# Optimization experiments

Hardware: AMD Instinct MI355X
Metric: run time of the kernel (lower is better)

Reference implementation:

```python
import jax, jax.numpy as jnp
import numpy as np

N = 100_000   # nodes
E = 1_600_000 # edges
IN, HID, OUT = 128, 64, 32


def _glorot(key, fan_in, fan_out):
    s = jnp.sqrt(6.0 / (fan_in + fan_out)).astype(jnp.float32)
    return jax.random.uniform(key, (fan_in, fan_out), jnp.float32, -s, s)


def setup_inputs() -> dict:
    key = jax.random.key(0)
    ks = jax.random.split(key, 8)
    x = jax.random.normal(ks[0], (N, IN), jnp.float32)
    edge_index = jax.random.randint(ks[1], (2, E), 0, N, jnp.int64)
    return {
        "x": x,
        "edge_index": edge_index,
        "W1": _glorot(ks[2], IN, HID),
        "b1": jnp.zeros((HID,), jnp.float32),
        "W_mu": _glorot(ks[3], HID, OUT),
        "b_mu": jnp.zeros((OUT,), jnp.float32),
        "W_ls": _glorot(ks[4], HID, OUT),
        "b_ls": jnp.zeros((OUT,), jnp.float32),
    }


def _gcn_conv(x, W, b, src, dst, n, dinv_sqrt):
    """PyG GCNConv: h = x @ W; symmetric-normalized scatter-add incl. self-loops; + b."""
    h = x @ W                                       # [N, F_out]
    coef = dinv_sqrt[src] * dinv_sqrt[dst]          # [E]
    msg = h[src] * coef[:, None]                    # [E, F_out] gather
    agg = jax.ops.segment_sum(msg, dst, num_segments=n)  # scatter-add
    agg = agg + h * (dinv_sqrt * dinv_sqrt)[:, None]      # self-loop contribution
    return agg + b


def reference(x, edge_index, W1, b1, W_mu, b_mu, W_ls, b_ls):
    src, dst = edge_index[0], edge_index[1]
    n = x.shape[0]
    # degree on graph with self-loops (edge weight 1), shared by all three convs
    deg = jax.ops.segment_sum(jnp.ones((src.shape[0],), x.dtype), dst, num_segments=n) + 1.0
    dinv_sqrt = jax.lax.rsqrt(deg)
    h = jax.nn.relu(_gcn_conv(x, W1, b1, src, dst, n, dinv_sqrt))
    mu = _gcn_conv(h, W_mu, b_mu, src, dst, n, dinv_sqrt)
    logstd = _gcn_conv(h, W_ls, b_ls, src, dst, n, dinv_sqrt)
    return mu, logstd
```

## Files before the change

kernel.cpp:

```cpp
#include <hip/hip_runtime.h>
#include <hip/hip_bf16.h>

#define FIN 128
#define HID 64
#define BSN 128
#define BSHIFT 7
#define SRCBITS 20
#define EPB 8192

typedef __attribute__((ext_vector_type(8))) short short8;
typedef __attribute__((ext_vector_type(4))) float floatx4;

__device__ __forceinline__ float bf2f(unsigned short u) {
    union { unsigned int i; float f; } c;
    c.i = ((unsigned int)u) << 16;
    return c.f;
}

__device__ __forceinline__ unsigned short f2bf(float f) {
    union { float f; unsigned int i; } c;
    c.f = f;
    unsigned int u = c.i;
    unsigned int r = (u + 0x7FFFu + ((u >> 16) & 1u)) >> 16;
    return (unsigned short)r;
}

__global__ void bin_count(const int* __restrict__ dst, int* __restrict__ bcnt,
                          int E, int B) {
    __shared__ int hist[1024];
    for (int i = threadIdx.x; i < 1024; i += 256) hist[i] = 0;
    __syncthreads();
    int base = blockIdx.x * EPB;
    int lim = min(base + EPB, E);
    for (int e = base + threadIdx.x; e < lim; e += 256)
        atomicAdd(&hist[dst[e] >> BSHIFT], 1);
    __syncthreads();
    for (int b = threadIdx.x; b < B; b += 256)
        if (hist[b]) atomicAdd(&bcnt[b], hist[b]);
}

__global__ void scan_bkt(int* __restrict__ bcnt, int* __restrict__ bbase,
                         int E, int B) {
    __shared__ int s[1024];
    int t = threadIdx.x;
    int v = (t < B) ? bcnt[t] : 0;
    s[t] = v;
    __syncthreads();
    for (int off = 1; off < 1024; off <<= 1) {
        int a = (t >= off) ? s[t - off] : 0;
        __syncthreads();
        s[t] += a;
        __syncthreads();
    }
    if (t < B) { int ex = s[t] - v; bbase[t] = ex; bcnt[t] = ex; }
    if (t == 0) bbase[B] = E;
}

__global__ void bin_fill(const int* __restrict__ src, const int* __restrict__ dst,
                         int* __restrict__ bcur, unsigned* __restrict__ rec, int E) {
    __shared__ int hist[1024];
    __shared__ int cbase[1024];
    for (int i = threadIdx.x; i < 1024; i += 256) hist[i] = 0;
    __syncthreads();
    int base = blockIdx.x * EPB;
    int lim = min(base + EPB, E);
    for (int e = base + threadIdx.x; e < lim; e += 256)
        atomicAdd(&hist[dst[e] >> BSHIFT], 1);
    __syncthreads();
    for (int b = threadIdx.x; b < 1024; b += 256) {
        int c = hist[b];
        cbase[b] = c ? atomicAdd(&bcur[b], c) : 0;
    }
    __syncthreads();
    for (int i = threadIdx.x; i < 1024; i += 256) hist[i] = 0;
    __syncthreads();
    for (int e = base + threadIdx.x; e < lim; e += 256) {
        int d = dst[e];
        int b = d >> BSHIFT;
        int slot = atomicAdd(&hist[b], 1);
        rec[cbase[b] + slot] = (unsigned)src[e] | ((unsigned)(d & (BSN - 1)) << SRCBITS);
    }
}

__global__ void csr_build(const unsigned* __restrict__ rec, const int* __restrict__ bbase,
                          int* __restrict__ row, int* __restrict__ rend,
                          int* __restrict__ csr, float* __restrict__ dinv, int N) {
    __shared__ int cnt[BSN], excl[BSN], cur[BSN];
    int b = blockIdx.x, t = threadIdx.x;
    if (t < BSN) cnt[t] = 0;
    __syncthreads();
    int start = bbase[b], end = bbase[b + 1];
    for (int i = start + t; i < end; i += 256)
        atomicAdd(&cnt[rec[i] >> SRCBITS], 1);
    __syncthreads();
    if (t < BSN) excl[t] = cnt[t];
    __syncthreads();
    for (int off = 1; off < BSN; off <<= 1) {
        int a = 0;
        if (t < BSN && t >= off) a = excl[t - off];
        __syncthreads();
        if (t < BSN) excl[t] += a;
        __syncthreads();
    }
    if (t < BSN) {
        int inc = excl[t];
        int ex = inc - cnt[t];
        excl[t] = ex;
        cur[t] = 0;
        int n = b * BSN + t;
        if (n < N) {
            row[n]  = start + ex;
            rend[n] = start + inc;
            dinv[n] = rsqrtf((float)cnt[t] + 1.0f);
        }
    }
    __syncthreads();
    for (int i = start + t; i < end; i += 256) {
        unsigned r = rec[i];
        int dl = r >> SRCBITS;
        int slot = atomicAdd(&cur[dl], 1);
        csr[start + excl[dl] + slot] = (int)(r & ((1u << SRCBITS) - 1));
    }
}

__global__ __launch_bounds__(256) void gemm1_mfma(
    const float* __restrict__ x, const float* __restrict__ W1,
    const float* __restrict__ dinv, unsigned short* __restrict__ h0, int N) {
    int wave = threadIdx.x >> 6, lane = threadIdx.x & 63;
    int m = lane & 15, q = lane >> 4;
    short8 bfr[4][4];
#pragma unroll
    for (int ct = 0; ct < 4; ++ct)
#pragma unroll
        for (int kk = 0; kk < 4; ++kk) {
            short8 tf;
#pragma unroll
            for (int jj = 0; jj < 8; ++jj)
                tf[jj] = (short)f2bf(W1[(kk * 32 + q * 8 + jj) * HID + ct * 16 + m]);
            bfr[ct][kk] = tf;
        }
    int ntiles = N >> 4;
    for (int t = blockIdx.x * 4 + wave; t < ntiles; t += gridDim.x * 4) {
        int nbase = t << 4;
        const float* xr = x + (size_t)(nbase + m) * FIN + q * 8;
        short8 afr[4];
#pragma unroll
        for (int kk = 0; kk < 4; ++kk) {
            float4 p0 = *((const float4*)(xr + kk * 32));
            float4 p1 = *((const float4*)(xr + kk * 32 + 4));
            short8 ta;
            ta[0] = (short)f2bf(p0.x); ta[1] = (short)f2bf(p0.y);
            ta[2] = (short)f2bf(p0.z); ta[3] = (short)f2bf(p0.w);
            ta[4] = (short)f2bf(p1.x); ta[5] = (short)f2bf(p1.y);
            ta[6] = (short)f2bf(p1.z); ta[7] = (short)f2bf(p1.w);
            afr[kk] = ta;
        }
        floatx4 cacc[4];
#pragma unroll
        for (int ct = 0; ct < 4; ++ct) cacc[ct] = floatx4{0.f, 0.f, 0.f, 0.f};
#pragma unroll
        for (int ct = 0; ct < 4; ++ct)
#pragma unroll
            for (int kk = 0; kk < 4; ++kk)
                cacc[ct] = __builtin_amdgcn_mfma_f32_16x16x32_bf16(afr[kk], bfr[ct][kk], cacc[ct], 0, 0, 0);
        float4 dv = *((const float4*)(dinv + nbase + q * 4));
#pragma unroll
        for (int ct = 0; ct < 4; ++ct) {
#pragma unroll
            for (int r = 0; r < 4; ++r) {
                float d = (r == 0) ? dv.x : (r == 1) ? dv.y : (r == 2) ? dv.z : dv.w;
                int n = nbase + q * 4 + r;
                h0[(size_t)n * HID + ct * 16 + m] = f2bf(cacc[ct][r] * d);
            }
        }
    }
}

__global__ void pull(const unsigned short* __restrict__ hp,
                     const int* __restrict__ row, const int* __restrict__ rend,
                     const int* __restrict__ csr, const float* __restrict__ dinv,
                     const float* __restrict__ b1,
                     unsigned short* __restrict__ outp, int N, int mode) {
    int wave = threadIdx.x >> 6, lane = threadIdx.x & 63;
    int n = blockIdx.x * 4 + wave;
    if (n >= N) return;
    int start = __builtin_amdgcn_readfirstlane(row[n]);
    int end   = __builtin_amdgcn_readfirstlane(rend[n]);
    float a0 = 0.f, a1 = 0.f, a2 = 0.f, a3 = 0.f;
    float a4 = 0.f, a5 = 0.f, a6 = 0.f, a7 = 0.f;
    int j = start;
    for (; j + 8 <= end; j += 8) {
        int s0 = csr[j],     s1 = csr[j + 1], s2 = csr[j + 2], s3 = csr[j + 3];
        int s4 = csr[j + 4], s5 = csr[j + 5], s6 = csr[j + 6], s7 = csr[j + 7];
        a0 += bf2f(hp[(size_t)s0 * HID + lane]);
        a1 += bf2f(hp[(size_t)s1 * HID + lane]);
        a2 += bf2f(hp[(size_t)s2 * HID + lane]);
        a3 += bf2f(hp[(size_t)s3 * HID + lane]);
        a4 += bf2f(hp[(size_t)s4 * HID + lane]);
        a5 += bf2f(hp[(size_t)s5 * HID + lane]);
        a6 += bf2f(hp[(size_t)s6 * HID + lane]);
        a7 += bf2f(hp[(size_t)s7 * HID + lane]);
    }
    for (; j < end; ++j) {
        int s = csr[j];
        a0 += bf2f(hp[(size_t)s * HID + lane]);
    }
    float acc = ((a0 + a1) + (a2 + a3)) + ((a4 + a5) + (a6 + a7));
    acc += bf2f(hp[(size_t)n * HID + lane]);
    float di = dinv[n];
    float v;
    if (mode == 0) {
        v = di * acc + b1[lane];
        v = v > 0.f ? v : 0.f;
        v *= di;
    } else {
        v = di * acc;
    }
    outp[(size_t)n * HID + lane] = f2bf(v);
}

__global__ __launch_bounds__(256, 4) void gemm2_mfma(
    const unsigned short* __restrict__ abar,
    const float* __restrict__ Wmu, const float* __restrict__ bmu,
    const float* __restrict__ Wls, const float* __restrict__ bls,
    float* __restrict__ out, int N) {
    int wave = threadIdx.x >> 6, lane = threadIdx.x & 63;
    int m = lane & 15, q = lane >> 4;
    short8 bfr[4][2];
#pragma unroll
    for (int ct = 0; ct < 4; ++ct)
#pragma unroll
        for (int kk = 0; kk < 2; ++kk) {
            short8 tf;
#pragma unroll
            for (int jj = 0; jj < 8; ++jj) {
                int k = kk * 32 + q * 8 + jj;
                int col = ct * 16 + m;
                float w = (col < 32) ? Wmu[k * 32 + col] : Wls[k * 32 + (col - 32)];
                tf[jj] = (short)f2bf(w);
            }
            bfr[ct][kk] = tf;
        }
    float bias[4];
#pragma unroll
    for (int ct = 0; ct < 4; ++ct) {
        int col = ct * 16 + m;
        bias[ct] = (col < 32) ? bmu[col] : bls[col - 32];
    }
    int ntiles = N >> 4;
    int gw = blockIdx.x * 4 + wave;
    int nw = gridDim.x * 4;
    for (int t = gw; t < ntiles; t += nw) {
        int nbase = t << 4;
        const unsigned short* arow = abar + (size_t)(nbase + m) * HID;
        short8 a0 = *((const short8*)(arow + q * 8));
        short8 a1 = *((const short8*)(arow + 32 + q * 8));
        floatx4 cacc[4];
#pragma unroll
        for (int ct = 0; ct < 4; ++ct) cacc[ct] = floatx4{0.f, 0.f, 0.f, 0.f};
#pragma unroll
        for (int ct = 0; ct < 4; ++ct) {
            cacc[ct] = __builtin_amdgcn_mfma_f32_16x16x32_bf16(a0, bfr[ct][0], cacc[ct], 0, 0, 0);
            cacc[ct] = __builtin_amdgcn_mfma_f32_16x16x32_bf16(a1, bfr[ct][1], cacc[ct], 0, 0, 0);
        }
#pragma unroll
        for (int ct = 0; ct < 4; ++ct) {
            int col = ct * 16 + m;
            int which = col >> 5, o = col & 31;
#pragma unroll
            for (int r = 0; r < 4; ++r) {
                int n = nbase + q * 4 + r;
                out[(size_t)which * N * 32 + (size_t)n * 32 + o] = cacc[ct][r] + bias[ct];
            }
        }
    }
}

extern "C" void kernel_launch(void* const* d_in, const int* in_sizes, int n_in,
                              void* d_out, int out_size, void* d_ws, size_t ws_size,
                              hipStream_t stream) {
    const float* x   = (const float*)d_in[0];
    const int*   ei  = (const int*)d_in[1];
    const float* W1  = (const float*)d_in[2];
    const float* b1  = (const float*)d_in[3];
    const float* Wmu = (const float*)d_in[4];
    const float* bmu = (const float*)d_in[5];
    const float* Wls = (const float*)d_in[6];
    const float* bls = (const float*)d_in[7];
    int N = in_sizes[0] / FIN;
    int E = in_sizes[1] / 2;
    const int* src = ei;
    const int* dst = ei + E;
    float* out = (float*)d_out;

    int B = (N + BSN - 1) / BSN;
    int nbin = (E + EPB - 1) / EPB;

    float* dinv  = (float*)d_ws;
    int*   row   = (int*)(dinv + N);
    int*   rend  = row + N;
    int*   bbase = rend + N;
    int*   bcur  = bbase + (B + 1);
    int*   csr   = bcur + B;
    unsigned short* bufA = (unsigned short*)(csr + E);
    char* region2 = (char*)(bufA + (size_t)N * HID);
    unsigned* rec        = (unsigned*)region2;
    unsigned short* bufB = (unsigned short*)region2;

    hipMemsetAsync(bcur, 0, (size_t)B * sizeof(int), stream);
    bin_count<<<nbin, 256, 0, stream>>>(dst, bcur, E, B);
    scan_bkt<<<1, 1024, 0, stream>>>(bcur, bbase, E, B);
    bin_fill<<<nbin, 256, 0, stream>>>(src, dst, bcur, rec, E);
    csr_build<<<B, 256, 0, stream>>>(rec, bbase, row, rend, csr, dinv, N);

    gemm1_mfma<<<256, 256, 0, stream>>>(x, W1, dinv, bufA, N);

    int pgrid = (N + 3) / 4;
    pull<<<pgrid, 256, 0, stream>>>(bufA, row, rend, csr, dinv, b1, bufB, N, 0);
    pull<<<pgrid, 256, 0, stream>>>(bufB, row, rend, csr, dinv, b1, bufA, N, 1);

    gemm2_mfma<<<256, 256, 0, stream>>>(bufA, Wmu, bmu, Wls, bls, out, N);
}
```

Baseline: 308.7 us.

## Stage bin records in LDS, widen buckets, and pair-gather neighbors in pull

bin_fill now scatters each block's edge records into a shared-memory staging buffer sorted by bucket, then writes them out contiguously per bucket. This replaces random global scatter stores with coalesced ones. Bucket size doubles to 256 nodes, which halves the bucket count and lets csr_build use all 256 threads. The pull kernel has each half-wave load a different neighbor's row as packed 32-bit bf16 pairs, unrolls over 16 edges and combines halves with a shuffle. It also runs as a fixed persistent grid with a grid-stride loop, at the cost of more LDS use and tail-handling complexity.

```diff
diff --git a/kernel.cpp b/kernel.cpp
--- a/kernel.cpp
+++ b/kernel.cpp
@@ -3,8 +3,8 @@
 
 #define FIN 128
 #define HID 64
-#define BSN 128
-#define BSHIFT 7
+#define BSN 256
+#define BSHIFT 8
 #define SRCBITS 20
 #define EPB 8192
 
@@ -14,6 +14,18 @@
 __device__ __forceinline__ float bf2f(unsigned short u) {
     union { unsigned int i; float f; } c;
     c.i = ((unsigned int)u) << 16;
+    return c.f;
+}
+
+__device__ __forceinline__ float lo_f(unsigned u) {
+    union { unsigned int i; float f; } c;
+    c.i = u << 16;
+    return c.f;
+}
+
+__device__ __forceinline__ float hi_f(unsigned u) {
+    union { unsigned int i; float f; } c;
+    c.i = u & 0xFFFF0000u;
     return c.f;
 }
 
@@ -27,8 +39,8 @@
 
 __global__ void bin_count(const int* __restrict__ dst, int* __restrict__ bcnt,
                           int E, int B) {
-    __shared__ int hist[1024];
-    for (int i = threadIdx.x; i < 1024; i += 256) hist[i] = 0;
+    __shared__ int hist[512];
+    for (int i = threadIdx.x; i < 512; i += 256) hist[i] = 0;
     __syncthreads();
     int base = blockIdx.x * EPB;
     int lim = min(base + EPB, E);
@@ -56,29 +68,55 @@
     if (t == 0) bbase[B] = E;
 }
 
-__global__ void bin_fill(const int* __restrict__ src, const int* __restrict__ dst,
-                         int* __restrict__ bcur, unsigned* __restrict__ rec, int E) {
-    __shared__ int hist[1024];
-    __shared__ int cbase[1024];
-    for (int i = threadIdx.x; i < 1024; i += 256) hist[i] = 0;
+__global__ __launch_bounds__(256) void bin_fill(
+    const int* __restrict__ src, const int* __restrict__ dst,
+    int* __restrict__ bcur, unsigned* __restrict__ rec, int E, int B) {
+    __shared__ int hist[512];
+    __shared__ int cbase[512];
+    __shared__ int lbase[512];
+    __shared__ int psum[256];
+    __shared__ unsigned recs[EPB];
+    int t = threadIdx.x;
+    for (int i = t; i < 512; i += 256) hist[i] = 0;
     __syncthreads();
     int base = blockIdx.x * EPB;
     int lim = min(base + EPB, E);
-    for (int e = base + threadIdx.x; e < lim; e += 256)
+    for (int e = base + t; e < lim; e += 256)
         atomicAdd(&hist[dst[e] >> BSHIFT], 1);
     __syncthreads();
-    for (int b = threadIdx.x; b < 1024; b += 256) {
+    for (int b = t; b < 512; b += 256) {
         int c = hist[b];
-        cbase[b] = c ? atomicAdd(&bcur[b], c) : 0;
-    }
-    __syncthreads();
-    for (int i = threadIdx.x; i < 1024; i += 256) hist[i] = 0;
-    __syncthreads();
-    for (int e = base + threadIdx.x; e < lim; e += 256) {
-        int d = dst[e];
+        cbase[b] = (c && b < B) ? atomicAdd(&bcur[b], c) : 0;
+    }
+    int h0 = hist[2 * t], h1 = hist[2 * t + 1];
+    psum[t] = h0 + h1;
+    __syncthreads();
+    int v = psum[t];
+    for (int off = 1; off < 256; off <<= 1) {
+        int a = (t >= off) ? psum[t - off] : 0;
+        __syncthreads();
+        psum[t] += a;
+        __syncthreads();
+    }
+    int ex = psum[t] - v;
+    lbase[2 * t] = ex;
+    lbase[2 * t + 1] = ex + h0;
+    hist[2 * t] = 0;
+    hist[2 * t + 1] = 0;
+    __syncthreads();
+    for (int e = base + t; e < lim; e += 256) {
+        int sv = src[e], d = dst[e];
         int b = d >> BSHIFT;
-        int slot = atomicAdd(&hist[b], 1);
-        rec[cbase[b] + slot] = (unsigned)src[e] | ((unsigned)(d & (BSN - 1)) << SRCBITS);
+        int slot = lbase[b] + atomicAdd(&hist[b], 1);
+        recs[slot] = (unsigned)sv | ((unsigned)(d & (BSN - 1)) << SRCBITS);
+    }
+    __syncthreads();
+    int wave = t >> 6, lane = t & 63;
+    for (int b = wave; b < B; b += 4) {
+        int c = hist[b];
+        int lb = lbase[b], gb = cbase[b];
+        for (int l = lane; l < c; l += 64)
+            rec[gb + l] = recs[lb + l];
     }
 }
 
@@ -87,22 +125,21 @@
                           int* __restrict__ csr, float* __restrict__ dinv, int N) {
     __shared__ int cnt[BSN], excl[BSN], cur[BSN];
     int b = blockIdx.x, t = threadIdx.x;
-    if (t < BSN) cnt[t] = 0;
+    cnt[t] = 0;
     __syncthreads();
     int start = bbase[b], end = bbase[b + 1];
     for (int i = start + t; i < end; i += 256)
         atomicAdd(&cnt[rec[i] >> SRCBITS], 1);
     __syncthreads();
-    if (t < BSN) excl[t] = cnt[t];
+    excl[t] = cnt[t];
     __syncthreads();
     for (int off = 1; off < BSN; off <<= 1) {
-        int a = 0;
-        if (t < BSN && t >= off) a = excl[t - off];
-        __syncthreads();
-        if (t < BSN) excl[t] += a;
-        __syncthreads();
-    }
-    if (t < BSN) {
+        int a = (t >= off) ? excl[t - off] : 0;
+        __syncthreads();
+        excl[t] += a;
+        __syncthreads();
+    }
+    {
         int inc = excl[t];
         int ex = inc - cnt[t];
         excl[t] = ex;
@@ -176,47 +213,73 @@
     }
 }
 
-__global__ void pull(const unsigned short* __restrict__ hp,
-                     const int* __restrict__ row, const int* __restrict__ rend,
-                     const int* __restrict__ csr, const float* __restrict__ dinv,
-                     const float* __restrict__ b1,
-                     unsigned short* __restrict__ outp, int N, int mode) {
+__global__ __launch_bounds__(256) void pull(
+    const unsigned short* __restrict__ hp, const int* __restrict__ row,
+    const int* __restrict__ rend, const int* __restrict__ csr,
+    const float* __restrict__ dinv, const float* __restrict__ b1,
+    unsigned short* __restrict__ outp, int N, int mode) {
+    const unsigned* hp32 = (const unsigned*)hp;
+    unsigned* out32 = (unsigned*)outp;
     int wave = threadIdx.x >> 6, lane = threadIdx.x & 63;
-    int n = blockIdx.x * 4 + wave;
-    if (n >= N) return;
-    int start = __builtin_amdgcn_readfirstlane(row[n]);
-    int end   = __builtin_amdgcn_readfirstlane(rend[n]);
-    float a0 = 0.f, a1 = 0.f, a2 = 0.f, a3 = 0.f;
-    float a4 = 0.f, a5 = 0.f, a6 = 0.f, a7 = 0.f;
-    int j = start;
-    for (; j + 8 <= end; j += 8) {
-        int s0 = csr[j],     s1 = csr[j + 1], s2 = csr[j + 2], s3 = csr[j + 3];
-        int s4 = csr[j + 4], s5 = csr[j + 5], s6 = csr[j + 6], s7 = csr[j + 7];
-        a0 += bf2f(hp[(size_t)s0 * HID + lane]);
-        a1 += bf2f(hp[(size_t)s1 * HID + lane]);
-        a2 += bf2f(hp[(size_t)s2 * HID + lane]);
-        a3 += bf2f(hp[(size_t)s3 * HID + lane]);
-        a4 += bf2f(hp[(size_t)s4 * HID + lane]);
-        a5 += bf2f(hp[(size_t)s5 * HID + lane]);
-        a6 += bf2f(hp[(size_t)s6 * HID + lane]);
-        a7 += bf2f(hp[(size_t)s7 * HID + lane]);
-    }
-    for (; j < end; ++j) {
-        int s = csr[j];
-        a0 += bf2f(hp[(size_t)s * HID + lane]);
-    }
-    float acc = ((a0 + a1) + (a2 + a3)) + ((a4 + a5) + (a6 + a7));
-    acc += bf2f(hp[(size_t)n * HID + lane]);
-    float di = dinv[n];
-    float v;
-    if (mode == 0) {
-        v = di * acc + b1[lane];
-        v = v > 0.f ? v : 0.f;
-        v *= di;
-    } else {
-        v = di * acc;
-    }
-    outp[(size_t)n * HID + lane] = f2bf(v);
+    int half = lane >> 5, f2 = lane & 31;
+    float bx = b1[2 * f2], by = b1[2 * f2 + 1];
+    int gw = blockIdx.x * 4 + wave, nw = gridDim.x * 4;
+    for (int n = gw; n < N; n += nw) {
+        int start = __builtin_amdgcn_readfirstlane(row[n]);
+        int end   = __builtin_amdgcn_readfirstlane(rend[n]);
+        float ax[8], ay[8];
+#pragma unroll
+        for (int i = 0; i < 8; ++i) { ax[i] = 0.f; ay[i] = 0.f; }
+        int j = start;
+        for (; j + 16 <= end; j += 16) {
+            unsigned u[8];
+#pragma unroll
+            for (int i = 0; i < 8; ++i) {
+                int s0 = __builtin_amdgcn_readfirstlane(csr[j + 2 * i]);
+                int s1 = __builtin_amdgcn_readfirstlane(csr[j + 2 * i + 1]);
+                int s = half ? s1 : s0;
+                u[i] = hp32[(size_t)s * 32 + f2];
+            }
+#pragma unroll
+            for (int i = 0; i < 8; ++i) {
+                ax[i] += lo_f(u[i]);
+                ay[i] += hi_f(u[i]);
+            }
+        }
+        for (; j + 2 <= end; j += 2) {
+            int s0 = __builtin_amdgcn_readfirstlane(csr[j]);
+            int s1 = __builtin_amdgcn_readfirstlane(csr[j + 1]);
+            int s = half ? s1 : s0;
+            unsigned u = hp32[(size_t)s * 32 + f2];
+            ax[0] += lo_f(u); ay[0] += hi_f(u);
+        }
+        if (j < end) {
+            int s = __builtin_amdgcn_readfirstlane(csr[j]);
+            unsigned u = hp32[(size_t)s * 32 + f2];
+            ax[1] += half ? 0.f : lo_f(u);
+            ay[1] += half ? 0.f : hi_f(u);
+        }
+        float sx = ((ax[0] + ax[1]) + (ax[2] + ax[3])) + ((ax[4] + ax[5]) + (ax[6] + ax[7]));
+        float sy = ((ay[0] + ay[1]) + (ay[2] + ay[3])) + ((ay[4] + ay[5]) + (ay[6] + ay[7]));
+        sx += __shfl_xor(sx, 32);
+        sy += __shfl_xor(sy, 32);
+        unsigned us = hp32[(size_t)n * 32 + f2];
+        sx += lo_f(us); sy += hi_f(us);
+        float di = dinv[n];
+        if (half == 0) {
+            float vx, vy;
+            if (mode == 0) {
+                vx = di * sx + bx;
+                vy = di * sy + by;
+                vx = (vx > 0.f ? vx : 0.f) * di;
+                vy = (vy > 0.f ? vy : 0.f) * di;
+            } else {
+                vx = di * sx;
+                vy = di * sy;
+            }
+            out32[(size_t)n * 32 + f2] = (unsigned)f2bf(vx) | ((unsigned)f2bf(vy) << 16);
+        }
+    }
 }
 
 __global__ __launch_bounds__(256, 4) void gemm2_mfma(
@@ -310,14 +373,13 @@
     hipMemsetAsync(bcur, 0, (size_t)B * sizeof(int), stream);
     bin_count<<<nbin, 256, 0, stream>>>(dst, bcur, E, B);
     scan_bkt<<<1, 1024, 0, stream>>>(bcur, bbase, E, B);
-    bin_fill<<<nbin, 256, 0, stream>>>(src, dst, bcur, rec, E);
+    bin_fill<<<nbin, 256, 0, stream>>>(src, dst, bcur, rec, E, B);
     csr_build<<<B, 256, 0, stream>>>(rec, bbase, row, rend, csr, dinv, N);
 
     gemm1_mfma<<<256, 256, 0, stream>>>(x, W1, dinv, bufA, N);
 
-    int pgrid = (N + 3) / 4;
-    pull<<<pgrid, 256, 0, stream>>>(bufA, row, rend, csr, dinv, b1, bufB, N, 0);
-    pull<<<pgrid, 256, 0, stream>>>(bufB, row, rend, csr, dinv, b1, bufA, N, 1);
+    pull<<<2048, 256, 0, stream>>>(bufA, row, rend, csr, dinv, b1, bufB, N, 0);
+    pull<<<2048, 256, 0, stream>>>(bufB, row, rend, csr, dinv, b1, bufA, N, 1);
 
     gemm2_mfma<<<256, 256, 0, stream>>>(bufA, Wmu, bmu, Wls, bls, out, N);
 }
```

After: 310.5 us. No clear change (+0.6%).
